# Kernel tuning notes

Measured on AMD Instinct MI355X. Metric: run time of the kernel, lower is better.

## Reference

```python
import jax, jax.numpy as jnp
import numpy as np

B = 2          # batch size
T2 = 9         # temporal groups (b*t2 = grid_sample batch)
T3 = 27        # t1 // t2
T1 = 243       # t2 * t3
P = 17         # joints
K2 = 9         # kernel_size ** 2
C = 128        # dim_img
CH = [48, 96, 192, 384]
HW = [(96, 72), (48, 36), (24, 18), (12, 9)]
ALPHA = 0.9


def setup_inputs() -> dict:
    key = jax.random.key(0)
    ks = jax.random.split(key, 16)
    inp = {}
    N = B * T2
    for i, (c, (h, w)) in enumerate(zip(CH, HW)):
        inp[f"f{i}"] = jax.random.normal(ks[i], (N, c, h, w), jnp.float32)
    inp["query"] = jax.random.normal(ks[4], (B, T1, P * K2, C), jnp.float32)
    # key holds normalized grid coords in [-1, 1]
    inp["key"] = jax.random.uniform(ks[5], (N, T3, P * K2, 2), jnp.float32) * 2.0 - 1.0
    inp["value"] = jax.random.normal(ks[6], (B, T1, P, C), jnp.float32)
    s = 0.05
    inp["w_off"] = jax.random.normal(ks[7], (2, C), jnp.float32) * s
    inp["b_off"] = jnp.zeros((2,), jnp.float32)
    inp["w_attn"] = jax.random.normal(ks[8], (2, C), jnp.float32) * s
    inp["b_attn"] = jnp.zeros((2,), jnp.float32)
    for i, c in enumerate(CH):
        inp[f"we{i}"] = jax.random.normal(ks[9 + i], (C, c), jnp.float32) * s
        inp[f"be{i}"] = jnp.zeros((C,), jnp.float32)
    inp["conv_w"] = jax.random.normal(ks[13], (C, C, K2), jnp.float32) * s
    inp["conv_b"] = jnp.zeros((C,), jnp.float32)
    return inp


def _grid_sample(img, grid):
    """Bilinear grid_sample, align_corners=False, zero padding.
    img: [N, C, H, W]; grid: [N, Hg, Wg, 2] in [-1,1] (x=width, y=height).
    Returns [N, Hg, Wg, C] (channels-last for the following 1x1 conv)."""
    N, Cin, H, W = img.shape
    gx, gy = grid[..., 0], grid[..., 1]
    ix = ((gx + 1.0) * W - 1.0) * 0.5
    iy = ((gy + 1.0) * H - 1.0) * 0.5
    ix0 = jnp.floor(ix); iy0 = jnp.floor(iy)
    wx1 = ix - ix0; wx0 = 1.0 - wx1
    wy1 = iy - iy0; wy0 = 1.0 - wy1
    bidx = jnp.arange(N)[:, None, None]

    def gather(yy, xx):
        yi = yy.astype(jnp.int32); xi = xx.astype(jnp.int32)
        valid = (yi >= 0) & (yi < H) & (xi >= 0) & (xi < W)
        yc = jnp.clip(yi, 0, H - 1); xc = jnp.clip(xi, 0, W - 1)
        v = img[bidx, :, yc, xc]  # [N, Hg, Wg, C]
        return v * valid[..., None].astype(img.dtype)

    out = (gather(iy0, ix0) * (wy0 * wx0)[..., None]
           + gather(iy0, ix0 + 1.0) * (wy0 * wx1)[..., None]
           + gather(iy0 + 1.0, ix0) * (wy1 * wx0)[..., None]
           + gather(iy0 + 1.0, ix0 + 1.0) * (wy1 * wx1)[..., None])
    return out


def reference(f0, f1, f2, f3, query, key, value,
              w_off, b_off, w_attn, b_attn,
              we0, be0, we1, be1, we2, be2, we3, be3,
              conv_w, conv_b):
    b, t1, p, c = value.shape            # [B, 243, 17, 128]
    t3 = key.shape[1]                    # 27
    t2 = t1 // t3                        # 9

    # learned offsets per query location, squashed by tanh
    off = jnp.tanh(jnp.einsum('btqc,oc->btqo', query, w_off) + b_off)   # [b,t1,153,2]
    # per-joint softmax weights, tiled over the k^2 kernel taps
    aw = jax.nn.softmax(jnp.einsum('btpc,oc->btpo', value, w_attn) + b_attn, axis=-1)  # [b,t1,17,2]
    aw = jnp.tile(aw, (1, 1, K2, 1))                                     # [b,t1,153,2]

    sp = (off * aw).reshape(b * t2, t3, p * K2, 2)
    sampling_positions = key + sp                                        # [b*t2, 27, 153, 2]

    fmaps = (f0, f1, f2, f3)
    ws = (we0, we1, we2, we3)
    bs = (be0, be1, be2, be3)
    feats = []
    for f, w, bb in zip(fmaps, ws, bs):
        g = _grid_sample(f, sampling_positions)                          # [b*t2, 27, 153, C_in]
        e = jnp.einsum('nhwc,oc->nhwo', g, w) + bb                        # 1x1 conv embed -> 128
        feats.append(e.reshape(b, t2 * t3, p * K2, C))                    # [b, 243, 153, 128]
    new_query = jnp.mean(jnp.stack(feats, axis=-2), axis=-2)             # fuse 4 levels
    new_query = (1.0 - ALPHA) * new_query + ALPHA * query

    # grouped-by-position conv1d over the k^2 taps (full-width kernel -> length 1)
    x = new_query.reshape(b, t1, p, K2, c)                               # 'b t (p k) c'
    new_value = jnp.einsum('btpkc,ock->btpo', x, conv_w) + conv_b        # [b, 243, 17, 128]
    return (new_query, new_value, sampling_positions)
```

## Files before the change

kernel.cpp:

```cpp
#include <hip/hip_runtime.h>
#include <hip/hip_bf16.h>

static constexpr int NQ_SIZE = 9517824;
static constexpr int NV_SIZE = 1057536;
static constexpr int NPOS    = 74358;
static constexpr int M_CONV  = 8262;

static constexpr long E0_OFF = 0;
static constexpr long E1_OFF = 15925248;
static constexpr long E2_OFF = E1_OFF + 3981312;
static constexpr long E3_OFF = E2_OFF + 995328;
static constexpr long E_END  = E3_OFF + 248832;

static constexpr int SEG_F3  = 36;
static constexpr int SEG_F2  = SEG_F3 + 126;
static constexpr int SEG_F1  = SEG_F2 + 486;
static constexpr int SEG_F0  = SEG_F1 + 1944;
static constexpr int SEG_CT  = SEG_F0 + 576;
static constexpr int SEG_SP  = SEG_CT + 486;
static constexpr int PREP_GRID = SEG_SP;

typedef __attribute__((ext_vector_type(8))) short short8;
typedef __attribute__((ext_vector_type(4))) float floatx4;

__device__ __forceinline__ float bf2f(unsigned short u) {
    union { unsigned int i; float f; } v; v.i = ((unsigned)u) << 16; return v.f;
}
__device__ __forceinline__ unsigned short f2bf_rne(float f) {
    union { float f; unsigned int i; } v; v.f = f;
    unsigned int u = v.i;
    u += 0x7fffu + ((u >> 16) & 1u);
    return (unsigned short)(u >> 16);
}

__global__ __launch_bounds__(256) void prep_k(
    const float* __restrict__ f0, const float* __restrict__ f1,
    const float* __restrict__ f2, const float* __restrict__ f3,
    const float* __restrict__ we0, const float* __restrict__ we1,
    const float* __restrict__ we2, const float* __restrict__ we3,
    const float* __restrict__ conv_w, unsigned short* __restrict__ convT2,
    const float* __restrict__ query, const float* __restrict__ value,
    const float* __restrict__ key,
    const float* __restrict__ w_off, const float* __restrict__ b_off,
    const float* __restrict__ w_attn, const float* __restrict__ b_attn,
    float* __restrict__ samp, unsigned short* __restrict__ Ebase)
{
    const int bid = blockIdx.x;
    const int tid = threadIdx.x;

    if (bid < SEG_F0) {
        __shared__ float As[16][64];
        __shared__ float Ws[16][128];
        const float* A; const float* W; unsigned short* Eo;
        int M, K, m0;
        if (bid < SEG_F3) {
            int n = bid >> 1, t = bid & 1;
            M = 108; K = 384; A = f3 + (long)n * 384 * 108; W = we3;
            Eo = Ebase + E3_OFF + (long)n * 108 * 128; m0 = t * 64;
        } else if (bid < SEG_F2) {
            int r = bid - SEG_F3; int n = r / 7, t = r - n * 7;
            M = 432; K = 192; A = f2 + (long)n * 192 * 432; W = we2;
            Eo = Ebase + E2_OFF + (long)n * 432 * 128; m0 = t * 64;
        } else if (bid < SEG_F1) {
            int r = bid - SEG_F2; int n = r / 27, t = r - n * 27;
            M = 1728; K = 96; A = f1 + (long)n * 96 * 1728; W = we1;
            Eo = Ebase + E1_OFF + (long)n * 1728 * 128; m0 = t * 64;
        } else {
            int r = bid - SEG_F1; int n = r / 108, t = r - n * 108;
            M = 6912; K = 48; A = f0 + (long)n * 48 * 6912; W = we0;
            Eo = Ebase + E0_OFF + (long)n * 6912 * 128; m0 = t * 64;
        }

        const int to = tid & 31;
        const int tm = tid >> 5;
        const int sk = tid >> 4;
        const int sm = (tid & 15) << 2;
        const int bo = tid >> 1;
        const int bh = (tid & 1) << 3;

        float acc[8][4];
        #pragma unroll
        for (int i = 0; i < 8; ++i)
            #pragma unroll
            for (int j = 0; j < 4; ++j) acc[i][j] = 0.f;

        float4 a_pf, b_pf0, b_pf1;
        auto fetch = [&](int k0) {
            a_pf = (float4){0.f, 0.f, 0.f, 0.f};
            if (m0 + sm < M)
                a_pf = *(const float4*)(A + (long)(k0 + sk) * M + m0 + sm);
            const float* wp = W + (long)bo * K + k0 + bh;
            b_pf0 = *(const float4*)wp;
            b_pf1 = *(const float4*)(wp + 4);
        };
        fetch(0);

        for (int k0 = 0; k0 < K; k0 += 16) {
            *(float4*)&As[sk][sm] = a_pf;
            Ws[bh + 0][bo] = b_pf0.x; Ws[bh + 1][bo] = b_pf0.y;
            Ws[bh + 2][bo] = b_pf0.z; Ws[bh + 3][bo] = b_pf0.w;
            Ws[bh + 4][bo] = b_pf1.x; Ws[bh + 5][bo] = b_pf1.y;
            Ws[bh + 6][bo] = b_pf1.z; Ws[bh + 7][bo] = b_pf1.w;
            __syncthreads();
            if (k0 + 16 < K) fetch(k0 + 16);
            #pragma unroll
            for (int k = 0; k < 16; ++k) {
                float4 a0 = *(const float4*)&As[k][tm * 8];
                float4 a1 = *(const float4*)&As[k][tm * 8 + 4];
                float am[8] = {a0.x, a0.y, a0.z, a0.w, a1.x, a1.y, a1.z, a1.w};
                float wv[4] = {Ws[k][to], Ws[k][to + 32], Ws[k][to + 64], Ws[k][to + 96]};
                #pragma unroll
                for (int mi = 0; mi < 8; ++mi)
                    #pragma unroll
                    for (int oi = 0; oi < 4; ++oi)
                        acc[mi][oi] = fmaf(am[mi], wv[oi], acc[mi][oi]);
            }
            __syncthreads();
        }

        #pragma unroll
        for (int mi = 0; mi < 8; ++mi) {
            int m = m0 + tm * 8 + mi;
            if (m < M) {
                #pragma unroll
                for (int oi = 0; oi < 4; ++oi)
                    Eo[(long)m * 128 + to + 32 * oi] = f2bf_rne(acc[mi][oi]);
            }
        }
    } else if (bid < SEG_CT) {
        int idx = (bid - SEG_F0) * 256 + tid;
        if (idx < 147456) {
            int o = idx / 1152, kk = idx - o * 1152;
            int k2 = kk >> 7, c = kk & 127;
            convT2[idx] = f2bf_rne(conv_w[o * 1152 + c * 9 + k2]);
        }
    } else {
        const int bt1 = bid - SEG_CT;
        const int b  = bt1 / 243, t1 = bt1 - b * 243;
        const int t2 = t1 / 27,  t3 = t1 - t2 * 27;
        const int n  = b * 9 + t2;
        __shared__ float logit[17][2];
        __shared__ float aw[17][2];

        if (tid < 34) {
            int p = tid >> 1, o = tid & 1;
            const float* vrow = value + ((long)bt1 * 17 + p) * 128;
            const float* wrow = w_attn + o * 128;
            float s = 0.f;
            for (int c = 0; c < 128; c += 4) {
                float4 v = *(const float4*)(vrow + c);
                float4 w = *(const float4*)(wrow + c);
                s += v.x * w.x + v.y * w.y + v.z * w.z + v.w * w.w;
            }
            logit[p][o] = s + b_attn[o];
        }
        __syncthreads();
        if (tid < 17) {
            float l0 = logit[tid][0], l1 = logit[tid][1];
            float mx = fmaxf(l0, l1);
            float e0 = expf(l0 - mx), e1 = expf(l1 - mx);
            float inv = 1.f / (e0 + e1);
            aw[tid][0] = e0 * inv; aw[tid][1] = e1 * inv;
        }
        __syncthreads();
        for (int j = tid; j < 306; j += 256) {
            int q = j >> 1, o = j & 1;
            const float* qrow = query + ((long)bt1 * 153 + q) * 128;
            const float* wrow = w_off + o * 128;
            float s = 0.f;
            for (int c = 0; c < 128; c += 4) {
                float4 v = *(const float4*)(qrow + c);
                float4 w = *(const float4*)(wrow + c);
                s += v.x * w.x + v.y * w.y + v.z * w.z + v.w * w.w;
            }
            float off = tanhf(s + b_off[o]);
            float sp = off * aw[q % 17][o];
            long kidx = (((long)n * 27 + t3) * 153 + q) * 2 + o;
            samp[kidx] = key[kidx] + sp;
        }
    }
}

__global__ __launch_bounds__(256) void gather_k(
    const unsigned short* __restrict__ Ebase,
    const float* __restrict__ samp, const float* __restrict__ query,
    const float* __restrict__ be0, const float* __restrict__ be1,
    const float* __restrict__ be2, const float* __restrict__ be3,
    float* __restrict__ nq)
{
    const int tid = threadIdx.x;
    const int pos = blockIdx.x * 8 + (tid >> 5);
    if (pos >= NPOS) return;
    const int c4 = (tid & 31) << 2;
    const int bt1 = pos / 153, q = pos - bt1 * 153;
    const int b  = bt1 / 243, t1 = bt1 - b * 243;
    const int t2 = t1 / 27,  t3 = t1 - t2 * 27;
    const int n  = b * 9 + t2;
    const long sbase = (((long)n * 27 + t3) * 153 + q) * 2;
    const float gx = samp[sbase], gy = samp[sbase + 1];

    float ax = 0.f, ay = 0.f, az = 0.f, aww = 0.f;
    const long Eoffs[4] = {E0_OFF, E1_OFF, E2_OFF, E3_OFF};
    const int Hs[4] = {96, 48, 24, 12}, Wd[4] = {72, 36, 18, 9};
    #pragma unroll
    for (int l = 0; l < 4; ++l) {
        const int H = Hs[l], W = Wd[l];
        const unsigned short* E = Ebase + Eoffs[l] + (long)n * H * W * 128 + c4;
        float ix = ((gx + 1.f) * (float)W - 1.f) * 0.5f;
        float iy = ((gy + 1.f) * (float)H - 1.f) * 0.5f;
        float fx0 = floorf(ix), fy0 = floorf(iy);
        int x0 = (int)fx0, y0 = (int)fy0;
        int x1 = x0 + 1, y1 = y0 + 1;
        float wx1 = ix - fx0, wx0 = 1.f - wx1;
        float wy1 = iy - fy0, wy0 = 1.f - wy1;
        float w00 = wy0 * wx0, w01 = wy0 * wx1, w10 = wy1 * wx0, w11 = wy1 * wx1;
        bool vy0 = (unsigned)y0 < (unsigned)H, vy1 = (unsigned)y1 < (unsigned)H;
        bool vx0 = (unsigned)x0 < (unsigned)W, vx1 = (unsigned)x1 < (unsigned)W;
        if (vy0 && vx0) { ushort4 v = *(const ushort4*)(E + ((long)y0 * W + x0) * 128);
            ax = fmaf(w00, bf2f(v.x), ax); ay = fmaf(w00, bf2f(v.y), ay);
            az = fmaf(w00, bf2f(v.z), az); aww = fmaf(w00, bf2f(v.w), aww); }
        if (vy0 && vx1) { ushort4 v = *(const ushort4*)(E + ((long)y0 * W + x1) * 128);
            ax = fmaf(w01, bf2f(v.x), ax); ay = fmaf(w01, bf2f(v.y), ay);
            az = fmaf(w01, bf2f(v.z), az); aww = fmaf(w01, bf2f(v.w), aww); }
        if (vy1 && vx0) { ushort4 v = *(const ushort4*)(E + ((long)y1 * W + x0) * 128);
            ax = fmaf(w10, bf2f(v.x), ax); ay = fmaf(w10, bf2f(v.y), ay);
            az = fmaf(w10, bf2f(v.z), az); aww = fmaf(w10, bf2f(v.w), aww); }
        if (vy1 && vx1) { ushort4 v = *(const ushort4*)(E + ((long)y1 * W + x1) * 128);
            ax = fmaf(w11, bf2f(v.x), ax); ay = fmaf(w11, bf2f(v.y), ay);
            az = fmaf(w11, bf2f(v.z), az); aww = fmaf(w11, bf2f(v.w), aww); }
    }
    float bsx = be0[c4]     + be1[c4]     + be2[c4]     + be3[c4];
    float bsy = be0[c4 + 1] + be1[c4 + 1] + be2[c4 + 1] + be3[c4 + 1];
    float bsz = be0[c4 + 2] + be1[c4 + 2] + be2[c4 + 2] + be3[c4 + 2];
    float bsw = be0[c4 + 3] + be1[c4 + 3] + be2[c4 + 3] + be3[c4 + 3];
    float mx = 0.25f * (ax + bsx), my = 0.25f * (ay + bsy);
    float mz = 0.25f * (az + bsz), mw = 0.25f * (aww + bsw);
    const long qi = ((long)bt1 * 153 + q) * 128 + c4;
    float4 qv = *(const float4*)(query + qi);
    float4 o;
    o.x = 0.1f * mx + 0.9f * qv.x;
    o.y = 0.1f * my + 0.9f * qv.y;
    o.z = 0.1f * mz + 0.9f * qv.z;
    o.w = 0.1f * mw + 0.9f * qv.w;
    *(float4*)(nq + qi) = o;
}

__global__ __launch_bounds__(256) void conv_mfma_k(
    const float* __restrict__ nq, const unsigned short* __restrict__ convT2,
    const float* __restrict__ conv_b, float* __restrict__ nv)
{
    __shared__ unsigned short As[64][40];
    __shared__ unsigned short Bs[64][40];

    const int tid  = threadIdx.x;
    const int lane = tid & 63;
    const int wave = tid >> 6;
    const int wm = (wave & 1) * 32;
    const int wn = (wave >> 1) * 32;
    const int m0 = blockIdx.x * 64;
    const int n0 = blockIdx.y * 64;
    const int l15  = lane & 15;
    const int quad = lane >> 4;

    floatx4 acc[2][2];
    #pragma unroll
    for (int i = 0; i < 2; ++i)
        #pragma unroll
        for (int j = 0; j < 2; ++j) acc[i][j] = (floatx4){0.f, 0.f, 0.f, 0.f};

    const int am = tid >> 2;
    const int ak = (tid & 3) << 3;
    const int bn = tid & 63;
    const int bk = (tid >> 6) << 3;

    float4 a0, a1; uint4 bv;
    auto fetch = [&](int k0) {
        a0 = (float4){0,0,0,0}; a1 = (float4){0,0,0,0};
        int row = m0 + am;
        if (row < M_CONV) {
            const float* p = nq + (long)row * 1152 + k0 + ak;
            a0 = *(const float4*)p;
            a1 = *(const float4*)(p + 4);
        }
        bv = *(const uint4*)(convT2 + (long)(n0 + bn) * 1152 + k0 + bk);
    };
    fetch(0);

    for (int k0 = 0; k0 < 1152; k0 += 32) {
        unsigned short* dst = &As[am][ak];
        dst[0] = f2bf_rne(a0.x); dst[1] = f2bf_rne(a0.y);
        dst[2] = f2bf_rne(a0.z); dst[3] = f2bf_rne(a0.w);
        dst[4] = f2bf_rne(a1.x); dst[5] = f2bf_rne(a1.y);
        dst[6] = f2bf_rne(a1.z); dst[7] = f2bf_rne(a1.w);
        *(uint4*)&Bs[bn][bk] = bv;
        __syncthreads();
        if (k0 + 32 < 1152) fetch(k0 + 32);

        short8 af[2], bfr[2];
        #pragma unroll
        for (int mt = 0; mt < 2; ++mt)
            af[mt] = *(const short8*)&As[wm + mt * 16 + l15][quad * 8];
        #pragma unroll
        for (int nt = 0; nt < 2; ++nt)
            bfr[nt] = *(const short8*)&Bs[wn + nt * 16 + l15][quad * 8];
        #pragma unroll
        for (int mt = 0; mt < 2; ++mt)
            #pragma unroll
            for (int nt = 0; nt < 2; ++nt)
                acc[mt][nt] = __builtin_amdgcn_mfma_f32_16x16x32_bf16(
                    af[mt], bfr[nt], acc[mt][nt], 0, 0, 0);
        __syncthreads();
    }

    #pragma unroll
    for (int mt = 0; mt < 2; ++mt) {
        #pragma unroll
        for (int nt = 0; nt < 2; ++nt) {
            int col = n0 + wn + nt * 16 + l15;
            float bias = conv_b[col];
            #pragma unroll
            for (int r = 0; r < 4; ++r) {
                int row = m0 + wm + mt * 16 + quad * 4 + r;
                if (row < M_CONV)
                    nv[(long)row * 128 + col] = acc[mt][nt][r] + bias;
            }
        }
    }
}

extern "C" void kernel_launch(void* const* d_in, const int* in_sizes, int n_in,
                              void* d_out, int out_size, void* d_ws, size_t ws_size,
                              hipStream_t stream) {
    const float* f0     = (const float*)d_in[0];
    const float* f1     = (const float*)d_in[1];
    const float* f2     = (const float*)d_in[2];
    const float* f3     = (const float*)d_in[3];
    const float* query  = (const float*)d_in[4];
    const float* key    = (const float*)d_in[5];
    const float* value  = (const float*)d_in[6];
    const float* w_off  = (const float*)d_in[7];
    const float* b_off  = (const float*)d_in[8];
    const float* w_attn = (const float*)d_in[9];
    const float* b_attn = (const float*)d_in[10];
    const float* we0    = (const float*)d_in[11];
    const float* be0    = (const float*)d_in[12];
    const float* we1    = (const float*)d_in[13];
    const float* be1    = (const float*)d_in[14];
    const float* we2    = (const float*)d_in[15];
    const float* be2    = (const float*)d_in[16];
    const float* we3    = (const float*)d_in[17];
    const float* be3    = (const float*)d_in[18];
    const float* conv_w = (const float*)d_in[19];
    const float* conv_b = (const float*)d_in[20];

    float* out  = (float*)d_out;
    float* nq   = out;
    float* nv   = out + NQ_SIZE;
    float* samp = out + NQ_SIZE + NV_SIZE;

    unsigned short* Ebase  = (unsigned short*)d_ws;
    unsigned short* convT2 = Ebase + E_END;

    prep_k<<<PREP_GRID, 256, 0, stream>>>(
        f0, f1, f2, f3, we0, we1, we2, we3, conv_w, convT2,
        query, value, key, w_off, b_off, w_attn, b_attn, samp, Ebase);

    gather_k<<<(NPOS + 7) / 8, 256, 0, stream>>>(Ebase, samp, query, be0, be1, be2, be3, nq);

    conv_mfma_k<<<dim3(130, 2), 256, 0, stream>>>(nq, convT2, conv_b, nv);
}
```

Baseline: 265.1 us.

## Use bf16 MFMA for per-level 1x1 embedding GEMM in prep kernel

Replaces the fp32 FMA register-tiled GEMM that projects each feature map level to 128 channels with a bf16 MFMA 16x16x32 path. Inputs and weights are converted to bf16 while being staged into padded shared-memory tiles, and the K step grows to 32. This targets the compute cost of the prep kernel's embedding segment, at the cost of rounding the inputs to bf16 before the multiply, which lowers accuracy, and a scattered transposed store into shared memory.

```diff
diff --git a/kernel.cpp b/kernel.cpp
--- a/kernel.cpp
+++ b/kernel.cpp
@@ -49,8 +49,9 @@
     const int tid = threadIdx.x;
 
     if (bid < SEG_F0) {
-        __shared__ float As[16][64];
-        __shared__ float Ws[16][128];
+        __shared__ unsigned short As[64][40];
+        __shared__ unsigned short Bs[128][40];
+
         const float* A; const float* W; unsigned short* Eo;
         int M, K, m0;
         if (bid < SEG_F3) {
@@ -71,60 +72,97 @@
             Eo = Ebase + E0_OFF + (long)n * 6912 * 128; m0 = t * 64;
         }
 
-        const int to = tid & 31;
-        const int tm = tid >> 5;
-        const int sk = tid >> 4;
-        const int sm = (tid & 15) << 2;
-        const int bo = tid >> 1;
-        const int bh = (tid & 1) << 3;
-
-        float acc[8][4];
-        #pragma unroll
-        for (int i = 0; i < 8; ++i)
-            #pragma unroll
-            for (int j = 0; j < 4; ++j) acc[i][j] = 0.f;
-
-        float4 a_pf, b_pf0, b_pf1;
+        const int lane = tid & 63;
+        const int wave = tid >> 6;
+        const int wm = (wave & 1) * 32;
+        const int wn = (wave >> 1) * 64;
+        const int l15  = lane & 15;
+        const int quad = lane >> 4;
+
+        floatx4 acc[2][4];
+        #pragma unroll
+        for (int i = 0; i < 2; ++i)
+            #pragma unroll
+            for (int j = 0; j < 4; ++j) acc[i][j] = (floatx4){0.f, 0.f, 0.f, 0.f};
+
+        const int sak = tid >> 3;
+        const int sam = (tid & 7) << 3;
+        const int sbo = tid >> 1;
+        const int sbk = (tid & 1) << 4;
+
+        float4 av0, av1, bv0, bv1, bv2, bv3;
         auto fetch = [&](int k0) {
-            a_pf = (float4){0.f, 0.f, 0.f, 0.f};
-            if (m0 + sm < M)
-                a_pf = *(const float4*)(A + (long)(k0 + sk) * M + m0 + sm);
-            const float* wp = W + (long)bo * K + k0 + bh;
-            b_pf0 = *(const float4*)wp;
-            b_pf1 = *(const float4*)(wp + 4);
+            av0 = (float4){0,0,0,0}; av1 = (float4){0,0,0,0};
+            if (k0 + sak < K) {
+                const float* p = A + (long)(k0 + sak) * M + m0 + sam;
+                if (m0 + sam + 7 < M) {
+                    av0 = *(const float4*)p;
+                    av1 = *(const float4*)(p + 4);
+                } else if (m0 + sam < M) {
+                    float tmp[8] = {0,0,0,0,0,0,0,0};
+                    int nv_ = M - (m0 + sam);
+                    for (int i = 0; i < 8; ++i) if (i < nv_) tmp[i] = p[i];
+                    av0 = (float4){tmp[0], tmp[1], tmp[2], tmp[3]};
+                    av1 = (float4){tmp[4], tmp[5], tmp[6], tmp[7]};
+                }
+            }
+            bv0 = (float4){0,0,0,0}; bv1 = bv0; bv2 = bv0; bv3 = bv0;
+            if (k0 + sbk < K) {
+                const float* wp = W + (long)sbo * K + k0 + sbk;
+                bv0 = *(const float4*)wp;
+                bv1 = *(const float4*)(wp + 4);
+                bv2 = *(const float4*)(wp + 8);
+                bv3 = *(const float4*)(wp + 12);
+            }
         };
         fetch(0);
 
-        for (int k0 = 0; k0 < K; k0 += 16) {
-            *(float4*)&As[sk][sm] = a_pf;
-            Ws[bh + 0][bo] = b_pf0.x; Ws[bh + 1][bo] = b_pf0.y;
-            Ws[bh + 2][bo] = b_pf0.z; Ws[bh + 3][bo] = b_pf0.w;
-            Ws[bh + 4][bo] = b_pf1.x; Ws[bh + 5][bo] = b_pf1.y;
-            Ws[bh + 6][bo] = b_pf1.z; Ws[bh + 7][bo] = b_pf1.w;
+        for (int k0 = 0; k0 < K; k0 += 32) {
+            {
+                float tmp[8] = {av0.x, av0.y, av0.z, av0.w, av1.x, av1.y, av1.z, av1.w};
+                #pragma unroll
+                for (int i = 0; i < 8; ++i)
+                    As[sam + i][sak] = f2bf_rne(tmp[i]);
+            }
+            {
+                unsigned short t[16];
+                float tmp[16] = {bv0.x, bv0.y, bv0.z, bv0.w, bv1.x, bv1.y, bv1.z, bv1.w,
+                                 bv2.x, bv2.y, bv2.z, bv2.w, bv3.x, bv3.y, bv3.z, bv3.w};
+                #pragma unroll
+                for (int i = 0; i < 16; ++i) t[i] = f2bf_rne(tmp[i]);
+                *(uint4*)&Bs[sbo][sbk]     = *(const uint4*)&t[0];
+                *(uint4*)&Bs[sbo][sbk + 8] = *(const uint4*)&t[8];
+            }
             __syncthreads();
-            if (k0 + 16 < K) fetch(k0 + 16);
-            #pragma unroll
-            for (int k = 0; k < 16; ++k) {
-                float4 a0 = *(const float4*)&As[k][tm * 8];
-                float4 a1 = *(const float4*)&As[k][tm * 8 + 4];
-                float am[8] = {a0.x, a0.y, a0.z, a0.w, a1.x, a1.y, a1.z, a1.w};
-                float wv[4] = {Ws[k][to], Ws[k][to + 32], Ws[k][to + 64], Ws[k][to + 96]};
+            if (k0 + 32 < K) fetch(k0 + 32);
+
+            short8 af[2], bfr[4];
+            #pragma unroll
+            for (int mt = 0; mt < 2; ++mt)
+                af[mt] = *(const short8*)&As[wm + mt * 16 + l15][quad * 8];
+            #pragma unroll
+            for (int nt = 0; nt < 4; ++nt)
+                bfr[nt] = *(const short8*)&Bs[wn + nt * 16 + l15][quad * 8];
+            #pragma unroll
+            for (int mt = 0; mt < 2; ++mt)
                 #pragma unroll
-                for (int mi = 0; mi < 8; ++mi)
-                    #pragma unroll
-                    for (int oi = 0; oi < 4; ++oi)
-                        acc[mi][oi] = fmaf(am[mi], wv[oi], acc[mi][oi]);
-            }
+                for (int nt = 0; nt < 4; ++nt)
+                    acc[mt][nt] = __builtin_amdgcn_mfma_f32_16x16x32_bf16(
+                        af[mt], bfr[nt], acc[mt][nt], 0, 0, 0);
             __syncthreads();
         }
 
         #pragma unroll
-        for (int mi = 0; mi < 8; ++mi) {
-            int m = m0 + tm * 8 + mi;
-            if (m < M) {
+        for (int mt = 0; mt < 2; ++mt) {
+            #pragma unroll
+            for (int nt = 0; nt < 4; ++nt) {
+                int col = wn + nt * 16 + l15;
                 #pragma unroll
-                for (int oi = 0; oi < 4; ++oi)
-                    Eo[(long)m * 128 + to + 32 * oi] = f2bf_rne(acc[mi][oi]);
+                for (int r = 0; r < 4; ++r) {
+                    int m = m0 + wm + mt * 16 + quad * 4 + r;
+                    if (m < M)
+                        Eo[(long)m * 128 + col] = f2bf_rne(acc[mt][nt][r]);
+                }
             }
         }
     } else if (bid < SEG_CT) {
```

New measurement: 246.9 us. -6.9%, faster.
